# Kernel tuning notes

Measured on AMD Instinct MI355X. Metric: run time of the kernel, lower is better.

## Reference

```python
import jax, jax.numpy as jnp
import numpy as np

N = 8000      # num_nodes
U = 64        # num_units
D = 2         # input_dim
K = 2         # max_diffusion_step
E = 64000     # edges per support
B = 32        # batch
F = D + U     # concat feature size = 66
M = 2 * K + 1 # num_matrices = 5


def setup_inputs() -> dict:
    key = jax.random.key(0)
    ks = jax.random.split(key, 10)
    return {
        "inputs": jax.random.normal(ks[0], (B, N * D), dtype=jnp.float32),
        "hx": jax.random.normal(ks[1], (B, N * U), dtype=jnp.float32),
        "row0": jax.random.randint(ks[2], (E,), 0, N, dtype=jnp.int32),
        "col0": jax.random.randint(ks[3], (E,), 0, N, dtype=jnp.int32),
        "val0": jax.random.uniform(ks[4], (E,), dtype=jnp.float32) / 8.0,
        "row1": jax.random.randint(ks[5], (E,), 0, N, dtype=jnp.int32),
        "col1": jax.random.randint(ks[6], (E,), 0, N, dtype=jnp.int32),
        "val1": jax.random.uniform(ks[7], (E,), dtype=jnp.float32) / 8.0,
        "W_ru": jax.random.normal(ks[8], (F * M, 2 * U), dtype=jnp.float32) * 0.05,
        "b_ru": jnp.ones((2 * U,), dtype=jnp.float32),  # bias_start=1.0
        "W_c": jax.random.normal(ks[9], (F * M, U), dtype=jnp.float32) * 0.05,
        "b_c": jnp.zeros((U,), dtype=jnp.float32),       # bias_start=0.0
    }


def _spmm(row, col, val, x):
    # y[r] += val_e * x[c]  for each edge e=(r,c); x: [N, F*B]
    return jax.ops.segment_sum(val[:, None] * x[col], row, num_segments=N)


def _gconv(inputs, state, W, b, supports, output_size):
    # inputs: [B, N*D_in], state: [B, N*D_st]
    x = jnp.concatenate([inputs.reshape(B, N, -1), state.reshape(B, N, -1)], axis=2)  # [B,N,F]
    f = x.shape[2]
    x0 = x.transpose(1, 2, 0).reshape(N, f * B)  # [N, F*B]
    xs = [x0]
    for (row, col, val) in supports:
        x1 = _spmm(row, col, val, x0)
        xs.append(x1)
        xk_1, xk_2 = x1, x0
        for _ in range(2, K + 1):
            x2 = 2.0 * _spmm(row, col, val, xk_1) - xk_2
            xs.append(x2)
            xk_1, xk_2 = x2, xk_1
    m = len(xs)
    # [M,N,F,B] -> [B,N,F,M] -> [B*N, F*M]
    xc = jnp.stack(xs).reshape(m, N, f, B).transpose(3, 1, 2, 0).reshape(B * N, f * m)
    out = xc @ W + b
    return out.reshape(B, N * output_size)


def reference(inputs, hx, row0, col0, val0, row1, col1, val1, W_ru, b_ru, W_c, b_c):
    supports = ((row0, col0, val0), (row1, col1, val1))
    # reset/update gates via graph convolution
    value = jax.nn.sigmoid(_gconv(inputs, hx, W_ru, b_ru, supports, 2 * U))
    value = value.reshape(B, N, 2 * U)
    r = value[..., :U].reshape(B, N * U)
    u = value[..., U:].reshape(B, N * U)
    c = jnp.tanh(_gconv(inputs, r * hx, W_c, b_c, supports, U))
    new_state = u * hx + (1.0 - u) * c
    return new_state
```

## Files before the change

### kernel.cpp

```cpp
#include <hip/hip_runtime.h>
#include <stdint.h>

#define NN 8000
#define UU 64
#define EE 64000
#define BB 32
#define NB 256000
#define HXS 512000

typedef __attribute__((ext_vector_type(8))) __bf16 bf16x8;
typedef __attribute__((ext_vector_type(4))) float f32x4;
typedef __attribute__((ext_vector_type(4))) unsigned int u32x4;

__device__ __forceinline__ unsigned short f2bf(float f){
  unsigned int u = __builtin_bit_cast(unsigned int, f);
  u += 0x7fffu + ((u >> 16) & 1u);
  return (unsigned short)(u >> 16);
}
__device__ __forceinline__ unsigned int pack2(float a, float b){
  return (unsigned int)f2bf(a) | ((unsigned int)f2bf(b) << 16);
}
__device__ __forceinline__ float bflo(unsigned int w){ return __builtin_bit_cast(float, w << 16); }
__device__ __forceinline__ float bfhi(unsigned int w){ return __builtin_bit_cast(float, w & 0xffff0000u); }
__device__ __forceinline__ float bfu(unsigned short v){ return __builtin_bit_cast(float, (unsigned int)v << 16); }

__device__ __forceinline__ void acc8(float* a, float v, uint4 q){
  a[0]+=v*bflo(q.x); a[1]+=v*bfhi(q.x); a[2]+=v*bflo(q.y); a[3]+=v*bfhi(q.y);
  a[4]+=v*bflo(q.z); a[5]+=v*bfhi(q.z); a[6]+=v*bfhi(q.w)*0.f + v*bflo(q.w); a[7]+=v*bfhi(q.w);
}

__device__ __forceinline__ void stage16(const unsigned short* g, unsigned short* ldsbase){
  __builtin_amdgcn_global_load_lds((const __attribute__((address_space(1))) void*)g,
                                   (__attribute__((address_space(3))) void*)ldsbase, 16, 0, 0);
}

__device__ __forceinline__ void ntstore16(uint4 v, uint4* p){
  u32x4 ov = {v.x, v.y, v.z, v.w};
  __builtin_nontemporal_store(ov, (u32x4*)p);
}

__global__ void k_hist(const int* __restrict__ r0, const int* __restrict__ r1, int* __restrict__ cnt){
  int i = blockIdx.x * 256 + threadIdx.x;
  if (i < 2*EE){
    int s = (i >= EE);
    int r = s ? r1[i - EE] : r0[i];
    atomicAdd(&cnt[s*NN + r], 1);
  }
}

__global__ __launch_bounds__(1024) void k_scan(const int* __restrict__ cnt, int* __restrict__ row_ptr, int* __restrict__ rp_work){
  int sup = blockIdx.x;
  const int* c = cnt + sup*NN;
  __shared__ int part[1024];
  int t = threadIdx.x;
  int loc[8]; int s = 0;
  #pragma unroll
  for (int j=0;j<8;j++){ int idx=t*8+j; int v = (idx<NN)? c[idx]:0; loc[j]=s; s+=v; }
  part[t]=s; __syncthreads();
  for (int o=1;o<1024;o<<=1){
    int v = (t>=o)? part[t-o]:0;
    __syncthreads();
    part[t]+=v;
    __syncthreads();
  }
  int pre = (t>0)? part[t-1]:0;
  #pragma unroll
  for (int j=0;j<8;j++){ int idx=t*8+j; if(idx<NN){ int e=pre+loc[j]; row_ptr[sup*(NN+1)+idx]=e; rp_work[sup*NN+idx]=e; } }
  if (t==1023) row_ptr[sup*(NN+1)+NN] = part[1023];
}

__global__ void k_scatter(const int* __restrict__ r0, const int* __restrict__ c0, const float* __restrict__ v0,
                          const int* __restrict__ r1, const int* __restrict__ c1, const float* __restrict__ v1,
                          int* __restrict__ rp_work, uint2* __restrict__ edge_s){
  int i = blockIdx.x * 256 + threadIdx.x;
  if (i < 2*EE){
    int s = (i >= EE);
    int e = s ? i - EE : i;
    int r  = s ? r1[e] : r0[e];
    int cc = s ? c1[e] : c0[e];
    float vv = s ? v1[e] : v0[e];
    int pos = atomicAdd(&rp_work[s*NN + r], 1);
    uint2 ev; ev.x = (unsigned int)cc; ev.y = __builtin_bit_cast(unsigned int, vv);
    edge_s[s*EE + pos] = ev;
  }
}

__global__ void k_wpack(const float* __restrict__ W_ru, const float* __restrict__ W_c,
                        unsigned short* __restrict__ Wru_t, unsigned short* __restrict__ Wc_t){
  int i = blockIdx.x * 256 + threadIdx.x;
  int k = i / 192; int oo = i % 192;
  const float* W; int ld, NC; unsigned short* dst; int c;
  if (oo < 128){ W = W_ru; ld = 128; NC = 128; dst = Wru_t; c = oo; }
  else         { W = W_c;  ld = 64;  NC = 64;  dst = Wc_t;  c = oo - 128; }
  int o = 4*(c & 15) + ((c >> 4) & 3);
  int wcol = (c >= 64) ? 64 + o : o;
  float v = 0.f;
  if (k < 330){
    int m, fb;
    if (k < 320){ m = k >> 6; fb = (2 + (k & 63)) * 5; }
    else        { int j = k - 320; m = j >> 1; fb = (j & 1) * 5; }
    if      (m==0) v = W[(fb+0)*ld+wcol] - W[(fb+2)*ld+wcol] - W[(fb+4)*ld+wcol];
    else if (m==1) v = W[(fb+1)*ld+wcol];
    else if (m==2) v = 2.f*W[(fb+2)*ld+wcol];
    else if (m==3) v = W[(fb+3)*ld+wcol];
    else           v = 2.f*W[(fb+4)*ld+wcol];
  }
  int dstoff;
  if (k < 320) dstoff = (k>>6)*NC*64 + c*64 + (k&63);
  else         dstoff = 320*NC + c*32 + (k-320);
  dst[dstoff] = f2bf(v);
}

__global__ void k_x0(const float* __restrict__ inputs, const float* __restrict__ hx,
                     uint4* __restrict__ xs0q, unsigned int* __restrict__ xi0){
  int n = blockIdx.x, t = threadIdx.x;
  int b = t >> 3, ug = t & 7;
  const float4 h0 = *(const float4*)(hx + (size_t)b*HXS + n*64 + ug*8);
  const float4 h1 = *(const float4*)(hx + (size_t)b*HXS + n*64 + ug*8 + 4);
  uint4 o;
  o.x = pack2(h0.x, h0.y); o.y = pack2(h0.z, h0.w);
  o.z = pack2(h1.x, h1.y); o.w = pack2(h1.z, h1.w);
  xs0q[(size_t)(b>>1)*(NN*16) + (size_t)n*16 + (b&1)*8 + ug] = o;
  if (t < 32){
    int bb = t;
    const float2 g = *(const float2*)(inputs + (size_t)bb*(NN*2) + n*2);
    xi0[(((size_t)(bb>>2)*NN) + n)*4 + (bb&3)] = pack2(g.x, g.y);
  }
}

template<bool WITH_IN, bool NTDST>
__global__ void k_spmm(const int* __restrict__ row_ptr, const uint2* __restrict__ edge_s,
                       uint4* xs4, uint4* xi4,
                       int srcA, int dstA, int srcB, int dstB){
  int bid = blockIdx.x;
  if (WITH_IN && bid >= 16000){
    int b2 = bid - 16000;
    int s = b2 & 7, supi = (b2 >> 3) & 1, chunk = b2 >> 4;
    int n = chunk*256 + threadIdx.x;
    if (n >= NN) return;
    int msrc = supi ? srcB : srcA, mdst = supi ? dstB : dstA;
    size_t sb = (size_t)(msrc*8 + s)*NN, db = (size_t)(mdst*8 + s)*NN;
    int beg = row_ptr[supi*(NN+1)+n], end = row_ptr[supi*(NN+1)+n+1];
    const uint2* es = edge_s + supi*EE;
    float ai[8] = {0.f,0.f,0.f,0.f,0.f,0.f,0.f,0.f};
    for (int e = beg; e < end; ++e){
      uint2 ev = es[e];
      float v = __builtin_bit_cast(float, ev.y);
      uint4 qi = xi4[sb + ev.x];
      acc8(ai, v, qi);
    }
    uint4 oi;
    oi.x = pack2(ai[0],ai[1]); oi.y = pack2(ai[2],ai[3]); oi.z = pack2(ai[4],ai[5]); oi.w = pack2(ai[6],ai[7]);
    if (NTDST) ntstore16(oi, &xi4[db + n]); else xi4[db + n] = oi;
    return;
  }
  int xcd = bid & 7;
  int seq = bid >> 3;
  int supi = (seq >= 1000) ? 1 : 0;
  int seq2 = seq - supi*1000;
  int slice = (seq2 < 500) ? xcd : (xcd + 8);
  int group = (seq2 < 500) ? seq2 : (seq2 - 500);
  int sub = threadIdx.x >> 4, lane = threadIdx.x & 15;
  int n = group*16 + sub;
  int msrc = supi ? srcB : srcA, mdst = supi ? dstB : dstA;
  size_t sS = (size_t)msrc*(NN*256) + (size_t)slice*(NN*16);
  size_t dS = (size_t)mdst*(NN*256) + (size_t)slice*(NN*16);
  int beg = row_ptr[supi*(NN+1)+n], end = row_ptr[supi*(NN+1)+n+1];
  const uint2* es = edge_s + supi*EE;

  float a[8] = {0.f,0.f,0.f,0.f,0.f,0.f,0.f,0.f};
  for (int e0 = beg; e0 < end; e0 += 8){
    unsigned int cc[8]; float vv[8]; uint4 q[8];
    #pragma unroll
    for (int j=0;j<8;j++){
      int idx = e0 + j;
      uint2 ev = es[idx < end ? idx : end-1];
      cc[j] = ev.x;
      vv[j] = (idx < end) ? __builtin_bit_cast(float, ev.y) : 0.f;
    }
    #pragma unroll
    for (int j=0;j<8;j++) q[j] = xs4[sS + (size_t)cc[j]*16 + lane];
    #pragma unroll
    for (int j=0;j<8;j++) acc8(a, vv[j], q[j]);
  }
  uint4 o;
  o.x = pack2(a[0],a[1]); o.y = pack2(a[2],a[3]); o.z = pack2(a[4],a[5]); o.w = pack2(a[6],a[7]);
  if (NTDST) ntstore16(o, &xs4[dS + (size_t)n*16 + lane]);
  else       xs4[dS + (size_t)n*16 + lane] = o;
}

template<int NCOL, bool IS_RU>
__global__ __launch_bounds__(256, 3) void k_gemm(unsigned short* xsS,
                                                 const unsigned int* __restrict__ xsI,
                                                 const unsigned short* __restrict__ Wp,
                                                 const float* __restrict__ bias,
                                                 const float* __restrict__ hx,
                                                 float* cout,
                                                 unsigned short* ubuf){
  constexpr int CF = NCOL / 16;
  __shared__ unsigned short Bl[2][NCOL*64];
  __shared__ unsigned short Bt[NCOL*32];
  const int t = threadIdx.x;
  const int wv = t >> 6;
  const int l = t & 63;
  const int lr = l & 15;
  const int lg = l >> 4;
  const int R0 = blockIdx.x * 128;

  auto stageB = [&](int m, int buf){
    #pragma unroll
    for (int i=0;i<NCOL*8/256;i++){
      int g = t + i*256;
      int rr = g >> 3, c = g & 7;
      const unsigned short* gp = Wp + (size_t)(m*NCOL + rr)*64 + ((c ^ (rr&7)) << 3);
      stage16(gp, &Bl[buf][(size_t)(i*256 + wv*64)*8]);
    }
  };

  size_t abase[2];
  #pragma unroll
  for (int rf=0; rf<2; rf++){
    int row = R0 + wv*32 + rf*16 + lr;
    int n = row >> 5, b = row & 31;
    abase[rf] = (size_t)(b>>1)*(NN*128) + (size_t)n*128 + (b&1)*64;
  }
  auto loadA = [&](int m, uint4* dst){
    #pragma unroll
    for (int ks=0; ks<2; ks++)
      #pragma unroll
      for (int rf=0; rf<2; rf++)
        dst[ks*2+rf] = *(const uint4*)(xsS + (size_t)m*(NN*2048) + abase[rf] + ks*32 + lg*8);
  };

  uint4 aC[4], aN[4];
  loadA(0, aC);
  uint4 aT[2];
  #pragma unroll
  for (int rf=0; rf<2; rf++){
    int row = R0 + wv*32 + rf*16 + lr;
    int n = row >> 5, b = row & 31;
    size_t ib = (((size_t)(b>>2))*NN + n)*4 + (b&3);
    unsigned int q0=0u,q1=0u,q2=0u,q3=0u;
    if (lg == 0){
      q0 = xsI[ib];
      q1 = xsI[(size_t)8*NN*4 + ib];
      q2 = xsI[(size_t)16*NN*4 + ib];
      q3 = xsI[(size_t)24*NN*4 + ib];
    } else if (lg == 1){
      q0 = xsI[(size_t)32*NN*4 + ib];
    }
    uint4 qq; qq.x=q0; qq.y=q1; qq.z=q2; qq.w=q3;
    aT[rf] = qq;
  }
  stageB(0, 0);
  {
    #pragma unroll
    for (int i=0;i<NCOL*4/256;i++){
      int g = t + i*256;
      int rr = g >> 2, c = g & 3;
      const unsigned short* gp = Wp + (size_t)320*NCOL + rr*32 + ((c ^ (rr&3)) << 3);
      stage16(gp, &Bt[(size_t)(i*256 + wv*64)*8]);
    }
  }
  __syncthreads();

  f32x4 acc[2][CF];
  const f32x4 zero = {0.f,0.f,0.f,0.f};
  #pragma unroll
  for (int rf=0; rf<2; rf++)
    #pragma unroll
    for (int cf=0; cf<CF; cf++) acc[rf][cf] = zero;

  #pragma unroll
  for (int m=0; m<5; m++){
    int cur = m & 1;
    if (m < 4){
      stageB(m+1, cur^1);
      loadA(m+1, aN);
    }
    #pragma unroll
    for (int ks=0; ks<2; ks++){
      #pragma unroll
      for (int cf=0; cf<CF; cf++){
        int col = cf*16 + lr;
        int chunk = (ks*4 + lg) ^ (col & 7);
        bf16x8 bv = __builtin_bit_cast(bf16x8, *(const uint4*)(&Bl[cur][col*64 + chunk*8]));
        acc[0][cf] = __builtin_amdgcn_mfma_f32_16x16x32_bf16(__builtin_bit_cast(bf16x8, aC[ks*2+0]), bv, acc[0][cf], 0, 0, 0);
        acc[1][cf] = __builtin_amdgcn_mfma_f32_16x16x32_bf16(__builtin_bit_cast(bf16x8, aC[ks*2+1]), bv, acc[1][cf], 0, 0, 0);
      }
    }
    __syncthreads();
    #pragma unroll
    for (int i=0;i<4;i++) aC[i] = aN[i];
  }

  #pragma unroll
  for (int cf=0; cf<CF; cf++){
    int col = cf*16 + lr;
    int chunk = lg ^ (col & 3);
    bf16x8 bv = __builtin_bit_cast(bf16x8, *(const uint4*)(&Bt[col*32 + chunk*8]));
    acc[0][cf] = __builtin_amdgcn_mfma_f32_16x16x32_bf16(__builtin_bit_cast(bf16x8, aT[0]), bv, acc[0][cf], 0, 0, 0);
    acc[1][cf] = __builtin_amdgcn_mfma_f32_16x16x32_bf16(__builtin_bit_cast(bf16x8, aT[1]), bv, acc[1][cf], 0, 0, 0);
  }

  #pragma unroll
  for (int rf=0; rf<2; rf++){
    #pragma unroll
    for (int reg=0; reg<4; reg++){
      int row = R0 + wv*32 + rf*16 + (lg << 2) + reg;
      int n = row >> 5, b = row & 31;
      size_t rowoff = (size_t)b*HXS + (size_t)n*UU;
      size_t slot0 = (size_t)(b>>1)*(NN*128) + (size_t)n*128 + (b&1)*64;
      int o0 = lr << 2;
      if constexpr (IS_RU){
        uint2 hv = *(const uint2*)(xsS + slot0 + o0);
        unsigned short rr4[4], uu4[4];
        #pragma unroll
        for (int cf=0; cf<4; cf++){
          int o = o0 + cf;
          float vr = acc[rf][cf][reg]   + bias[o];
          float vu = acc[rf][cf+4][reg] + bias[64+o];
          float sgr = 1.f/(1.f + __expf(-vr));
          float sgu = 1.f/(1.f + __expf(-vu));
          float h = bfu(((const unsigned short*)&hv)[cf]);
          rr4[cf] = f2bf(sgr * h);
          uu4[cf] = f2bf(sgu);
        }
        *(uint2*)(xsS + slot0 + o0) = *(uint2*)rr4;
        *(uint2*)(ubuf + rowoff + o0) = *(uint2*)uu4;
      } else {
        float4 hv = *(const float4*)(hx + rowoff + o0);
        uint2 uv = *(const uint2*)(ubuf + rowoff + o0);
        float4 ov;
        #pragma unroll
        for (int cf=0; cf<4; cf++){
          float cc = tanhf(acc[rf][cf][reg] + bias[o0+cf]);
          float uu = bfu(((const unsigned short*)&uv)[cf]);
          float h  = ((const float*)&hv)[cf];
          ((float*)&ov)[cf] = uu*h + (1.f - uu)*cc;
        }
        *(float4*)(cout + rowoff + o0) = ov;
      }
    }
  }
}

extern "C" void kernel_launch(void* const* d_in, const int* in_sizes, int n_in,
                              void* d_out, int out_size, void* d_ws, size_t ws_size,
                              hipStream_t stream){
  const float* inputs = (const float*)d_in[0];
  const float* hx     = (const float*)d_in[1];
  const int*   row0   = (const int*)d_in[2];
  const int*   col0   = (const int*)d_in[3];
  const float* val0   = (const float*)d_in[4];
  const int*   row1   = (const int*)d_in[5];
  const int*   col1   = (const int*)d_in[6];
  const float* val1   = (const float*)d_in[7];
  const float* W_ru   = (const float*)d_in[8];
  const float* b_ru   = (const float*)d_in[9];
  const float* W_c    = (const float*)d_in[10];
  const float* b_c    = (const float*)d_in[11];
  float* out = (float*)d_out;

  char* ws = (char*)d_ws;
  size_t off = 0;
  auto alloc = [&](size_t bytes) -> void* {
    void* p = ws + off;
    off += (bytes + 255) & ~(size_t)255;
    return p;
  };
  unsigned short* xsS   = (unsigned short*)alloc((size_t)5*NN*2048*2);
  unsigned int*   xsI   = (unsigned int*)  alloc((size_t)5*8*NN*16);
  unsigned short* u_buf = (unsigned short*)alloc((size_t)NB*64*2);
  unsigned short* Wru_t = (unsigned short*)alloc((size_t)128*352*2);
  unsigned short* Wc_t  = (unsigned short*)alloc((size_t)64*352*2);
  int*   row_ptr = (int*)  alloc(2*(NN+1)*4);
  uint2* edge_s  = (uint2*)alloc((size_t)2*EE*8);
  int*   cnt     = (int*)  alloc(2*NN*4);
  int*   rp_work = (int*)  alloc(2*NN*4);
  (void)ws_size; (void)in_sizes; (void)n_in; (void)out_size;

  hipMemsetAsync(cnt, 0, 2*NN*4, stream);
  k_hist<<<(2*EE + 255)/256, 256, 0, stream>>>(row0, row1, cnt);
  k_scan<<<2, 1024, 0, stream>>>(cnt, row_ptr, rp_work);
  k_scatter<<<(2*EE + 255)/256, 256, 0, stream>>>(row0, col0, val0, row1, col1, val1, rp_work, edge_s);
  k_wpack<<<(352*192)/256, 256, 0, stream>>>(W_ru, W_c, Wru_t, Wc_t);
  k_x0<<<NN, 256, 0, stream>>>(inputs, hx, (uint4*)xsS, (unsigned int*)xsI);

  uint4* xs4 = (uint4*)xsS;
  uint4* xi4 = (uint4*)xsI;

  k_spmm<true , false><<<16512, 256, 0, stream>>>(row_ptr, edge_s, xs4, xi4, 0, 1, 0, 3);
  k_spmm<true , true ><<<16512, 256, 0, stream>>>(row_ptr, edge_s, xs4, xi4, 1, 2, 3, 4);
  k_gemm<128, true><<<2000, 256, 0, stream>>>(xsS, xsI, Wru_t, b_ru, hx, nullptr, u_buf);

  k_spmm<false, false><<<16000, 256, 0, stream>>>(row_ptr, edge_s, xs4, xi4, 0, 1, 0, 3);
  k_spmm<false, true ><<<16000, 256, 0, stream>>>(row_ptr, edge_s, xs4, xi4, 1, 2, 3, 4);
  k_gemm<64, false><<<2000, 256, 0, stream>>>(xsS, xsI, Wc_t, b_c, hx, out, u_buf);
}
```

Measured before the change: 451.8 us.

## Store state features node-major and process one node per wavefront in SpMM

The state buffer is reorganized from batch-pair slices into a contiguous per-node layout of 32 batches by 64 units, and the gemm addressing is updated to match. The SpMM now assigns a whole wavefront to one node, loads each neighbor's full 4 KB row with wide loads, and software-prefetches the next edge. This replaces 16 separate slice passes per edge with one contiguous gather, cutting repeated edge-list reads and improving locality. The cost is 32 accumulators per lane, a serial edge loop per wave with less memory-level parallelism, and loss of the previous XCD-aware slice scheduling for L2 reuse.

```diff
diff --git a/kernel.cpp b/kernel.cpp
--- a/kernel.cpp
+++ b/kernel.cpp
@@ -26,7 +26,7 @@
 
 __device__ __forceinline__ void acc8(float* a, float v, uint4 q){
   a[0]+=v*bflo(q.x); a[1]+=v*bfhi(q.x); a[2]+=v*bflo(q.y); a[3]+=v*bfhi(q.y);
-  a[4]+=v*bflo(q.z); a[5]+=v*bfhi(q.z); a[6]+=v*bfhi(q.w)*0.f + v*bflo(q.w); a[7]+=v*bfhi(q.w);
+  a[4]+=v*bflo(q.z); a[5]+=v*bfhi(q.z); a[6]+=v*bflo(q.w); a[7]+=v*bfhi(q.w);
 }
 
 __device__ __forceinline__ void stage16(const unsigned short* g, unsigned short* ldsbase){
@@ -120,7 +120,7 @@
   uint4 o;
   o.x = pack2(h0.x, h0.y); o.y = pack2(h0.z, h0.w);
   o.z = pack2(h1.x, h1.y); o.w = pack2(h1.z, h1.w);
-  xs0q[(size_t)(b>>1)*(NN*16) + (size_t)n*16 + (b&1)*8 + ug] = o;
+  xs0q[((size_t)n*32 + b)*8 + ug] = o;
   if (t < 32){
     int bb = t;
     const float2 g = *(const float2*)(inputs + (size_t)bb*(NN*2) + n*2);
@@ -128,13 +128,13 @@
   }
 }
 
-template<bool WITH_IN, bool NTDST>
-__global__ void k_spmm(const int* __restrict__ row_ptr, const uint2* __restrict__ edge_s,
-                       uint4* xs4, uint4* xi4,
-                       int srcA, int dstA, int srcB, int dstB){
+template<bool WITH_IN>
+__global__ __launch_bounds__(256) void k_spmm(const int* __restrict__ row_ptr, const uint2* __restrict__ edge_s,
+                                              unsigned short* xsS, uint4* xi4,
+                                              int srcA, int dstA, int srcB, int dstB){
   int bid = blockIdx.x;
-  if (WITH_IN && bid >= 16000){
-    int b2 = bid - 16000;
+  if (WITH_IN && bid >= 4000){
+    int b2 = bid - 4000;
     int s = b2 & 7, supi = (b2 >> 3) & 1, chunk = b2 >> 4;
     int n = chunk*256 + threadIdx.x;
     if (n >= NN) return;
@@ -151,42 +151,56 @@
     }
     uint4 oi;
     oi.x = pack2(ai[0],ai[1]); oi.y = pack2(ai[2],ai[3]); oi.z = pack2(ai[4],ai[5]); oi.w = pack2(ai[6],ai[7]);
-    if (NTDST) ntstore16(oi, &xi4[db + n]); else xi4[db + n] = oi;
+    if (supi) ntstore16(oi, &xi4[db + n]); else xi4[db + n] = oi;
     return;
   }
-  int xcd = bid & 7;
-  int seq = bid >> 3;
-  int supi = (seq >= 1000) ? 1 : 0;
-  int seq2 = seq - supi*1000;
-  int slice = (seq2 < 500) ? xcd : (xcd + 8);
-  int group = (seq2 < 500) ? seq2 : (seq2 - 500);
-  int sub = threadIdx.x >> 4, lane = threadIdx.x & 15;
-  int n = group*16 + sub;
+  int w = bid*4 + (threadIdx.x >> 6);
+  w = __builtin_amdgcn_readfirstlane(w);
+  int supi = (w >= NN) ? 1 : 0;
+  int n = w - supi*NN;
+  int lane = threadIdx.x & 63;
+  int lo = lane*8;
   int msrc = supi ? srcB : srcA, mdst = supi ? dstB : dstA;
-  size_t sS = (size_t)msrc*(NN*256) + (size_t)slice*(NN*16);
-  size_t dS = (size_t)mdst*(NN*256) + (size_t)slice*(NN*16);
-  int beg = row_ptr[supi*(NN+1)+n], end = row_ptr[supi*(NN+1)+n+1];
+  const unsigned short* srcS = xsS + (size_t)msrc*(NN*2048);
+  unsigned short* dstS = xsS + (size_t)mdst*(NN*2048);
+  int beg = __builtin_amdgcn_readfirstlane(row_ptr[supi*(NN+1)+n]);
+  int end = __builtin_amdgcn_readfirstlane(row_ptr[supi*(NN+1)+n+1]);
   const uint2* es = edge_s + supi*EE;
 
-  float a[8] = {0.f,0.f,0.f,0.f,0.f,0.f,0.f,0.f};
-  for (int e0 = beg; e0 < end; e0 += 8){
-    unsigned int cc[8]; float vv[8]; uint4 q[8];
-    #pragma unroll
-    for (int j=0;j<8;j++){
-      int idx = e0 + j;
-      uint2 ev = es[idx < end ? idx : end-1];
-      cc[j] = ev.x;
-      vv[j] = (idx < end) ? __builtin_bit_cast(float, ev.y) : 0.f;
-    }
-    #pragma unroll
-    for (int j=0;j<8;j++) q[j] = xs4[sS + (size_t)cc[j]*16 + lane];
-    #pragma unroll
-    for (int j=0;j<8;j++) acc8(a, vv[j], q[j]);
-  }
-  uint4 o;
-  o.x = pack2(a[0],a[1]); o.y = pack2(a[2],a[3]); o.z = pack2(a[4],a[5]); o.w = pack2(a[6],a[7]);
-  if (NTDST) ntstore16(o, &xs4[dS + (size_t)n*16 + lane]);
-  else       xs4[dS + (size_t)n*16 + lane] = o;
+  float a[32];
+  #pragma unroll
+  for (int i=0;i<32;i++) a[i] = 0.f;
+
+  uint4 qc[4]; float vc = 0.f;
+  if (beg < end){
+    uint2 ev = es[beg];
+    vc = __builtin_bit_cast(float, ev.y);
+    const unsigned short* rp = srcS + (size_t)ev.x*2048;
+    #pragma unroll
+    for (int c=0;c<4;c++) qc[c] = *(const uint4*)(rp + lo + c*512);
+  }
+  for (int e = beg; e < end; ++e){
+    uint4 qn[4]; float vn = 0.f;
+    if (e+1 < end){
+      uint2 ev = es[e+1];
+      vn = __builtin_bit_cast(float, ev.y);
+      const unsigned short* rp = srcS + (size_t)ev.x*2048;
+      #pragma unroll
+      for (int c=0;c<4;c++) qn[c] = *(const uint4*)(rp + lo + c*512);
+    }
+    #pragma unroll
+    for (int c=0;c<4;c++) acc8(a + c*8, vc, qc[c]);
+    #pragma unroll
+    for (int c=0;c<4;c++) qc[c] = qn[c];
+    vc = vn;
+  }
+  #pragma unroll
+  for (int c=0;c<4;c++){
+    uint4 o;
+    o.x = pack2(a[c*8+0],a[c*8+1]); o.y = pack2(a[c*8+2],a[c*8+3]);
+    o.z = pack2(a[c*8+4],a[c*8+5]); o.w = pack2(a[c*8+6],a[c*8+7]);
+    ntstore16(o, (uint4*)(dstS + (size_t)n*2048 + lo + c*512));
+  }
 }
 
 template<int NCOL, bool IS_RU>
@@ -219,11 +233,8 @@
 
   size_t abase[2];
   #pragma unroll
-  for (int rf=0; rf<2; rf++){
-    int row = R0 + wv*32 + rf*16 + lr;
-    int n = row >> 5, b = row & 31;
-    abase[rf] = (size_t)(b>>1)*(NN*128) + (size_t)n*128 + (b&1)*64;
-  }
+  for (int rf=0; rf<2; rf++)
+    abase[rf] = (size_t)(R0 + wv*32 + rf*16 + lr)*64;
   auto loadA = [&](int m, uint4* dst){
     #pragma unroll
     for (int ks=0; ks<2; ks++)
@@ -310,7 +321,7 @@
       int row = R0 + wv*32 + rf*16 + (lg << 2) + reg;
       int n = row >> 5, b = row & 31;
       size_t rowoff = (size_t)b*HXS + (size_t)n*UU;
-      size_t slot0 = (size_t)(b>>1)*(NN*128) + (size_t)n*128 + (b&1)*64;
+      size_t slot0 = (size_t)row*64;
       int o0 = lr << 2;
       if constexpr (IS_RU){
         uint2 hv = *(const uint2*)(xsS + slot0 + o0);
@@ -387,14 +398,13 @@
   k_wpack<<<(352*192)/256, 256, 0, stream>>>(W_ru, W_c, Wru_t, Wc_t);
   k_x0<<<NN, 256, 0, stream>>>(inputs, hx, (uint4*)xsS, (unsigned int*)xsI);
 
-  uint4* xs4 = (uint4*)xsS;
   uint4* xi4 = (uint4*)xsI;
 
-  k_spmm<true , false><<<16512, 256, 0, stream>>>(row_ptr, edge_s, xs4, xi4, 0, 1, 0, 3);
-  k_spmm<true , true ><<<16512, 256, 0, stream>>>(row_ptr, edge_s, xs4, xi4, 1, 2, 3, 4);
+  k_spmm<true ><<<4512, 256, 0, stream>>>(row_ptr, edge_s, xsS, xi4, 0, 1, 0, 3);
+  k_spmm<true ><<<4512, 256, 0, stream>>>(row_ptr, edge_s, xsS, xi4, 1, 2, 3, 4);
   k_gemm<128, true><<<2000, 256, 0, stream>>>(xsS, xsI, Wru_t, b_ru, hx, nullptr, u_buf);
 
-  k_spmm<false, false><<<16000, 256, 0, stream>>>(row_ptr, edge_s, xs4, xi4, 0, 1, 0, 3);
-  k_spmm<false, true ><<<16000, 256, 0, stream>>>(row_ptr, edge_s, xs4, xi4, 1, 2, 3, 4);
+  k_spmm<false><<<4000, 256, 0, stream>>>(row_ptr, edge_s, xsS, xi4, 0, 1, 0, 3);
+  k_spmm<false><<<4000, 256, 0, stream>>>(row_ptr, edge_s, xsS, xi4, 1, 2, 3, 4);
   k_gemm<64, false><<<2000, 256, 0, stream>>>(xsS, xsI, Wc_t, b_c, hx, out, u_buf);
 }
```

Result: slower. 511.7 us (+13.3%).
